# Optimization experiments

Hardware: AMD Instinct MI355X
Metric: run time of the kernel (lower is better)

Reference implementation:

```python
import jax, jax.numpy as jnp
import numpy as np


def setup_inputs() -> dict:
    key = jax.random.key(0)
    ks = jax.random.split(key, 8)
    B, D, H, W = 4, 96, 64, 64
    K, N, R = 4, 16, 6
    return {
        "x": jax.random.normal(ks[0], (B, D, H, W), jnp.float32),
        "x_proj_weight": jax.random.normal(ks[1], (K, R + 2 * N, D), jnp.float32) * 0.05,
        "dt_projs_weight": jax.random.normal(ks[2], (K, D, R), jnp.float32) * 0.1,
        "dt_projs_bias": jax.random.normal(ks[3], (K, D), jnp.float32) * 0.1,
        "A_logs": jax.random.uniform(ks[4], (K * D, N), jnp.float32),
        "Ds": jax.random.normal(ks[5], (K * D,), jnp.float32),
        "ln_weight": jnp.ones((D,), jnp.float32),
        "ln_bias": jnp.zeros((D,), jnp.float32),
    }


def reference(x, x_proj_weight, dt_projs_weight, dt_projs_bias, A_logs, Ds, ln_weight, ln_bias):
    B, D, H, W = x.shape
    K, _, R = dt_projs_weight.shape
    N = A_logs.shape[1]
    L = H * W

    # ---- CrossScan: 4 traversal orders (row-major, col-major, and their reverses) ----
    xf = x.reshape(B, D, L)                                   # row-major
    xt = jnp.transpose(x, (0, 1, 3, 2)).reshape(B, D, L)      # col-major
    xs = jnp.stack([xf, xt, xf[..., ::-1], xt[..., ::-1]], axis=1)  # (B, K, D, L)

    # ---- input-dependent projections ----
    x_dbl = jnp.einsum('bkdl,kcd->bkcl', xs, x_proj_weight)   # (B, K, R+2N, L)
    dts, Bs, Cs = jnp.split(x_dbl, [R, R + N], axis=2)        # Bs/Cs: (B, K, N, L)
    dts = jnp.einsum('bkrl,kdr->bkdl', dts, dt_projs_weight)  # (B, K, D, L)

    A = -jnp.exp(A_logs).reshape(K, D, N)                     # (K, D, N)
    delta = jax.nn.softplus(dts + dt_projs_bias[None, :, :, None])  # (B, K, D, L)

    # ---- selective (S6) scan over L ----
    def step(h, inp):
        d_t, u_t, B_t, C_t = inp  # (B,K,D) (B,K,D) (B,K,N) (B,K,N)
        dA = jnp.exp(d_t[..., None] * A[None])                # (B,K,D,N)
        h = h * dA + (d_t * u_t)[..., None] * B_t[:, :, None, :]
        y_t = jnp.einsum('bkdn,bkn->bkd', h, C_t)
        return h, y_t

    h0 = jnp.zeros((B, K, D, N), x.dtype)
    seq = (jnp.moveaxis(delta, -1, 0), jnp.moveaxis(xs, -1, 0),
           jnp.moveaxis(Bs, -1, 0), jnp.moveaxis(Cs, -1, 0))
    _, ys = jax.lax.scan(step, h0, seq)                       # (L, B, K, D)
    ys = jnp.moveaxis(ys, 0, -1)                              # (B, K, D, L)
    ys = ys + Ds.reshape(K, D)[None, :, :, None] * xs         # skip term D*u

    # ---- CrossMerge: undo the 4 traversal orders and sum ----
    m = ys[:, 0:2] + ys[:, 2:4][..., ::-1]                    # (B, 2, D, L)
    y = m[:, 0] + jnp.transpose(m[:, 1].reshape(B, D, W, H), (0, 1, 3, 2)).reshape(B, D, L)

    # ---- out_norm (LayerNorm over channels, v0 path) ----
    y = jnp.transpose(y, (0, 2, 1))                           # (B, L, D)
    mu = y.mean(-1, keepdims=True)
    var = y.var(-1, keepdims=True)
    y = (y - mu) / jnp.sqrt(var + 1e-5) * ln_weight + ln_bias
    return y.reshape(B, H, W, D)
```

## Files before the change

### kernel.cpp

```cpp
#include <hip/hip_runtime.h>
#include <math.h>

#define B_ 4
#define D_ 96
#define H_ 64
#define W_ 64
#define L_ 4096
#define K_ 4
#define N_ 16
#define R_ 6
#define C_ 38
#define SSX 128
#define CLSX (L_ / SSX)
#define CH_ (B_ * K_ * D_ * N_)

__device__ __forceinline__ int src_idx(int k, int l) {
    int m = (k >= 2) ? (L_ - 1 - l) : l;
    if (k & 1) return ((m & 63) << 6) | (m >> 6);
    return m;
}

__device__ __forceinline__ float softplus_f(float a) {
    return (a > 15.f) ? a : __logf(1.f + __expf(a));
}

__global__ __launch_bounds__(256) void transpose_kernel(
    const float* __restrict__ x,
    float* __restrict__ xs2)
{
    int bid = blockIdx.x;
    int b = bid / (3 * 64);
    int rest = bid % (3 * 64);
    int dblk = rest / 64, lblk = rest % 64;
    int d0 = dblk * 32;
    int l0 = lblk * 64;
    int tid = threadIdx.x;

    __shared__ float s_t[32][65];

    for (int i = tid; i < 32 * 64; i += 256) {
        int d = i >> 6, l = i & 63;
        s_t[d][l] = x[((long)b * D_ + d0 + d) * L_ + l0 + l];
    }
    __syncthreads();

    for (int i = tid; i < 64 * 32; i += 256) {
        int l = i >> 5, d = i & 31;
        float v = s_t[d][l];
        xs2[((long)b * L_ + l0 + l) * D_ + d0 + d] = v;
        xs2[((long)(B_ + b) * L_ + l * 64 + lblk) * D_ + d0 + d] = v;
    }
}

__global__ __launch_bounds__(256) void proj_kernel(
    const float* __restrict__ xs2,
    const float* __restrict__ xpw,
    const float* __restrict__ wdt,
    const float* __restrict__ bdt,
    float* __restrict__ delta,
    float* __restrict__ Bsb,
    float* __restrict__ Csb)
{
    const int TL = 64;
    const int tiles = L_ / TL;
    int bid = blockIdx.x;
    int bk = bid / tiles;
    int tile = bid % tiles;
    int b = bk / K_, k = bk % K_;
    int l0 = tile * TL;
    int tid = threadIdx.x;

    __shared__ __align__(16) float s_wpT[D_ * 40];
    __shared__ __align__(16) float s_xs[D_ * 68];
    __shared__ __align__(16) float s_wdt[R_ * D_];
    __shared__ __align__(16) float s_bias[D_];
    __shared__ __align__(16) float s_dts[R_ * 68];

    for (int i = tid; i < C_ * D_; i += 256) {
        int d = i / C_, c = i % C_;
        int cp = (c < 6) ? c : c + 2;
        s_wpT[d * 40 + cp] = xpw[(k * C_ + c) * D_ + d];
    }
    for (int i = tid; i < 96; i += 256) {
        s_wpT[i * 40 + 6] = 0.f;
        s_wpT[i * 40 + 7] = 0.f;
    }
    for (int i = tid; i < R_ * D_; i += 256) {
        int r = i / D_, d = i % D_;
        s_wdt[i] = wdt[(k * D_ + d) * R_ + r];
    }
    if (tid < D_) s_bias[tid] = bdt[k * D_ + tid];

    const float* xsp = xs2 + (long)((k & 1) * B_ + b) * L_ * D_;
    for (int i = tid; i < TL * 24; i += 256) {
        int lt = i / 24, dq = i % 24;
        int row = (k < 2) ? (l0 + lt) : (L_ - 1 - l0 - lt);
        float4 v = *(const float4*)(xsp + (long)row * D_ + dq * 4);
        s_xs[(dq * 4 + 0) * 68 + lt] = v.x;
        s_xs[(dq * 4 + 1) * 68 + lt] = v.y;
        s_xs[(dq * 4 + 2) * 68 + lt] = v.z;
        s_xs[(dq * 4 + 3) * 68 + lt] = v.w;
    }
    __syncthreads();

    long base = (long)bk * L_ + l0;

    int ct = tid >> 4;
    int lt4 = (tid & 15) * 4;
    if (ct < 10) {
        int cp0 = ct * 4;
        float acc[4][4];
#pragma unroll
        for (int i = 0; i < 4; ++i)
#pragma unroll
            for (int j = 0; j < 4; ++j) acc[i][j] = 0.f;
#pragma unroll 4
        for (int d = 0; d < D_; ++d) {
            float4 wv = *(const float4*)(&s_wpT[d * 40 + cp0]);
            float4 xv = *(const float4*)(&s_xs[d * 68 + lt4]);
            float wa[4] = {wv.x, wv.y, wv.z, wv.w};
            float xa[4] = {xv.x, xv.y, xv.z, xv.w};
#pragma unroll
            for (int ci = 0; ci < 4; ++ci)
#pragma unroll
                for (int li = 0; li < 4; ++li)
                    acc[ci][li] += wa[ci] * xa[li];
        }
        if (ct == 0) {
#pragma unroll
            for (int ci = 0; ci < 4; ++ci)
                *(float4*)(&s_dts[ci * 68 + lt4]) =
                    make_float4(acc[ci][0], acc[ci][1], acc[ci][2], acc[ci][3]);
        } else if (ct == 1) {
#pragma unroll
            for (int ci = 0; ci < 2; ++ci)
                *(float4*)(&s_dts[(4 + ci) * 68 + lt4]) =
                    make_float4(acc[ci][0], acc[ci][1], acc[ci][2], acc[ci][3]);
        } else if (ct < 6) {
            int n0 = cp0 - 8;
#pragma unroll
            for (int li = 0; li < 4; ++li)
                *(float4*)(&Bsb[(base + lt4 + li) * N_ + n0]) =
                    make_float4(acc[0][li], acc[1][li], acc[2][li], acc[3][li]);
        } else {
            int n0 = cp0 - 24;
#pragma unroll
            for (int li = 0; li < 4; ++li)
                *(float4*)(&Csb[(base + lt4 + li) * N_ + n0]) =
                    make_float4(acc[0][li], acc[1][li], acc[2][li], acc[3][li]);
        }
    }
    __syncthreads();

    for (int tt = tid; tt < 24 * 16; tt += 256) {
        int dt = tt % 24, lt4b = (tt / 24) * 4;
        int d0 = dt * 4;
        float4 bias = *(const float4*)(&s_bias[d0]);
        float acc[4][4];
#pragma unroll
        for (int li = 0; li < 4; ++li) {
            acc[li][0] = bias.x; acc[li][1] = bias.y;
            acc[li][2] = bias.z; acc[li][3] = bias.w;
        }
#pragma unroll
        for (int r = 0; r < R_; ++r) {
            float4 wv = *(const float4*)(&s_wdt[r * D_ + d0]);
            float4 tv = *(const float4*)(&s_dts[r * 68 + lt4b]);
            float wa[4] = {wv.x, wv.y, wv.z, wv.w};
            float ta[4] = {tv.x, tv.y, tv.z, tv.w};
#pragma unroll
            for (int li = 0; li < 4; ++li)
#pragma unroll
                for (int di = 0; di < 4; ++di)
                    acc[li][di] += ta[li] * wa[di];
        }
#pragma unroll
        for (int li = 0; li < 4; ++li) {
            float4 o = make_float4(softplus_f(acc[li][0]), softplus_f(acc[li][1]),
                                   softplus_f(acc[li][2]), softplus_f(acc[li][3]));
            *(float4*)(&delta[(base + lt4b + li) * D_ + d0]) = o;
        }
    }
}

__global__ __launch_bounds__(192) void scan_part1(
    const float* __restrict__ A_logs,
    const float* __restrict__ xs2,
    const float* __restrict__ delta,
    const float* __restrict__ Bsb,
    float* __restrict__ pAarr,
    float* __restrict__ hharr)
{
    int cid = blockIdx.x * 2 + threadIdx.x / 96;
    int dd = threadIdx.x % 96;
    int bk = cid / SSX;
    int j = cid % SSX;
    int b = bk / K_, k = bk % K_;
    int kd = k * D_ + dd;
    int l0 = j * CLSX;

    float Av[16];
    {
        const float4* ap = (const float4*)(A_logs + kd * N_);
#pragma unroll
        for (int q = 0; q < 4; ++q) {
            float4 a = ap[q];
            Av[q * 4 + 0] = -__expf(a.x); Av[q * 4 + 1] = -__expf(a.y);
            Av[q * 4 + 2] = -__expf(a.z); Av[q * 4 + 3] = -__expf(a.w);
        }
    }

    const float* dp = delta + ((long)bk * L_ + l0) * D_ + dd;
    const float* bp = Bsb + ((long)bk * L_ + l0) * N_;
    const float* xsp = xs2 + (long)((k & 1) * B_ + b) * L_ * D_;
    long urow0 = (k < 2) ? l0 : (L_ - 1 - l0);
    long ustep = (k < 2) ? D_ : -D_;
    const float* up = xsp + urow0 * D_ + dd;

    float h[16], pA[16];
#pragma unroll
    for (int i = 0; i < 16; ++i) { h[i] = 0.f; pA[i] = 1.f; }

#pragma unroll 2
    for (int t = 0; t < CLSX; ++t) {
        float del = dp[t * D_];
        float u   = up[t * ustep];
        float Bv[16];
        *(float4*)(Bv + 0)  = *(const float4*)(bp + t * N_);
        *(float4*)(Bv + 4)  = *(const float4*)(bp + t * N_ + 4);
        *(float4*)(Bv + 8)  = *(const float4*)(bp + t * N_ + 8);
        *(float4*)(Bv + 12) = *(const float4*)(bp + t * N_ + 12);
        float delu = del * u;
#pragma unroll
        for (int i = 0; i < 16; ++i) {
            float dA = __expf(del * Av[i]);
            pA[i] *= dA;
            h[i] = h[i] * dA + delu * Bv[i];
        }
    }

    long sbase = (long)j * CH_ + (long)(bk * D_ + dd) * N_;
#pragma unroll
    for (int q = 0; q < 4; ++q) {
        *(float4*)(pAarr + sbase + q * 4) =
            make_float4(pA[q * 4], pA[q * 4 + 1], pA[q * 4 + 2], pA[q * 4 + 3]);
        *(float4*)(hharr + sbase + q * 4) =
            make_float4(h[q * 4], h[q * 4 + 1], h[q * 4 + 2], h[q * 4 + 3]);
    }
}

__global__ __launch_bounds__(256) void scan_combine(
    const float* __restrict__ pAarr,
    float* __restrict__ hharr)
{
    int c = blockIdx.x * 256 + threadIdx.x;
    float h = 0.f;
#pragma unroll 8
    for (int j = 0; j < SSX; ++j) {
        long idx = (long)j * CH_ + c;
        float tmp = hharr[idx];
        float pa  = pAarr[idx];
        hharr[idx] = h;
        h = tmp + pa * h;
    }
}

__global__ __launch_bounds__(192) void scan_part2_pair(
    const float* __restrict__ A_logs,
    const float* __restrict__ Ds,
    const float* __restrict__ xs2,
    const float* __restrict__ delta,
    const float* __restrict__ Bsb,
    const float* __restrict__ Csb,
    const float* __restrict__ hharr,
    float* __restrict__ ypair)
{
    __shared__ float s_y[2][CLSX][D_];

    int bid = blockIdx.x;
    int b = bid / (2 * SSX);
    int rest = bid % (2 * SSX);
    int p = rest / SSX;
    int j = rest % SSX;
    int tid = threadIdx.x;
    int g = tid / 96;
    int dd = tid % 96;

    int kdir = p + 2 * g;
    int bk = b * K_ + kdir;
    int jj = g ? (SSX - 1 - j) : j;
    int l0s = jj * CLSX;
    int kd = kdir * D_ + dd;

    float Av[16];
    {
        const float4* ap = (const float4*)(A_logs + kd * N_);
#pragma unroll
        for (int q = 0; q < 4; ++q) {
            float4 a = ap[q];
            Av[q * 4 + 0] = -__expf(a.x); Av[q * 4 + 1] = -__expf(a.y);
            Av[q * 4 + 2] = -__expf(a.z); Av[q * 4 + 3] = -__expf(a.w);
        }
    }
    float Dv = Ds[kd];

    const float* dp = delta + ((long)bk * L_ + l0s) * D_ + dd;
    const float* bp = Bsb + ((long)bk * L_ + l0s) * N_;
    const float* cp = Csb + ((long)bk * L_ + l0s) * N_;
    const float* xsp = xs2 + (long)(p * B_ + b) * L_ * D_;
    long urow0 = g ? ((long)j * CLSX + CLSX - 1) : (long)l0s;
    long ustep = g ? -D_ : D_;
    const float* up = xsp + urow0 * D_ + dd;

    float h[16];
    {
        long sbase = (long)jj * CH_ + (long)(bk * D_ + dd) * N_;
#pragma unroll
        for (int q = 0; q < 4; ++q) {
            float4 hv = *(const float4*)(hharr + sbase + q * 4);
            h[q * 4] = hv.x; h[q * 4 + 1] = hv.y;
            h[q * 4 + 2] = hv.z; h[q * 4 + 3] = hv.w;
        }
    }

#pragma unroll 2
    for (int t = 0; t < CLSX; ++t) {
        float del = dp[t * D_];
        float u   = up[t * ustep];
        float Bv[16], Cv[16];
        *(float4*)(Bv + 0)  = *(const float4*)(bp + t * N_);
        *(float4*)(Bv + 4)  = *(const float4*)(bp + t * N_ + 4);
        *(float4*)(Bv + 8)  = *(const float4*)(bp + t * N_ + 8);
        *(float4*)(Bv + 12) = *(const float4*)(bp + t * N_ + 12);
        *(float4*)(Cv + 0)  = *(const float4*)(cp + t * N_);
        *(float4*)(Cv + 4)  = *(const float4*)(cp + t * N_ + 4);
        *(float4*)(Cv + 8)  = *(const float4*)(cp + t * N_ + 8);
        *(float4*)(Cv + 12) = *(const float4*)(cp + t * N_ + 12);
        float delu = del * u;
        float yv = 0.f;
#pragma unroll
        for (int i = 0; i < 16; ++i) {
            float dA = __expf(del * Av[i]);
            h[i] = h[i] * dA + delu * Bv[i];
            yv += h[i] * Cv[i];
        }
        int tpos = g ? (CLSX - 1 - t) : t;
        s_y[g][tpos][dd] = yv + Dv * u;
    }
    __syncthreads();

    float* yo = ypair + ((long)(p * B_ + b) * L_ + (long)j * CLSX) * D_;
    for (int i = tid; i < CLSX * 24; i += 192) {
        int lt = i / 24, dq = i % 24;
        int d0 = dq * 4;
        float4 o = make_float4(s_y[0][lt][d0 + 0] + s_y[1][lt][d0 + 0],
                               s_y[0][lt][d0 + 1] + s_y[1][lt][d0 + 1],
                               s_y[0][lt][d0 + 2] + s_y[1][lt][d0 + 2],
                               s_y[0][lt][d0 + 3] + s_y[1][lt][d0 + 3]);
        *(float4*)(yo + (long)lt * D_ + d0) = o;
    }
}

__global__ __launch_bounds__(256) void ln_merge_kernel(
    const float* __restrict__ ypair,
    const float* __restrict__ lnw,
    const float* __restrict__ lnb,
    float* __restrict__ out)
{
    int wid = (blockIdx.x * 256 + threadIdx.x) >> 6;
    int lane = threadIdx.x & 63;
    int b = wid / L_;
    int m = wid % L_;
    int mt = ((m & 63) << 6) | (m >> 6);

    const float* y0 = ypair + ((long)b * L_ + m) * D_;
    const float* y1 = ypair + ((long)(B_ + b) * L_ + mt) * D_;

    float v0 = y0[lane] + y1[lane];
    float v1 = (lane < 32) ? (y0[64 + lane] + y1[64 + lane]) : 0.f;

    float s  = v0 + v1;
    float s2 = v0 * v0 + v1 * v1;
#pragma unroll
    for (int mm = 1; mm < 64; mm <<= 1) {
        s  += __shfl_xor(s, mm);
        s2 += __shfl_xor(s2, mm);
    }
    float mu  = s * (1.f / D_);
    float var = s2 * (1.f / D_) - mu * mu;
    float rstd = rsqrtf(var + 1e-5f);

    long obase = (long)wid * D_;
    out[obase + lane] = (v0 - mu) * rstd * lnw[lane] + lnb[lane];
    if (lane < 32)
        out[obase + 64 + lane] = (v1 - mu) * rstd * lnw[64 + lane] + lnb[64 + lane];
}

__global__ __launch_bounds__(256) void proj_legacy(
    const float* __restrict__ x,
    const float* __restrict__ xpw,
    const float* __restrict__ wdt,
    const float* __restrict__ bdt,
    float* __restrict__ delta,
    float* __restrict__ Bsb,
    float* __restrict__ Csb)
{
    const int TL = 64;
    const int tiles = L_ / TL;
    int bid = blockIdx.x;
    int bk = bid / tiles;
    int tile = bid % tiles;
    int b = bk / K_, k = bk % K_;
    int l0 = tile * TL;
    int tid = threadIdx.x;

    __shared__ float s_wp[C_ * D_];
    __shared__ float s_wdt[R_ * D_];
    __shared__ float s_bias[D_];
    __shared__ float s_xs[D_ * (TL + 1)];
    __shared__ float s_xdbl[C_ * (TL + 1)];

    for (int i = tid; i < C_ * D_; i += 256) s_wp[i] = xpw[k * C_ * D_ + i];
    for (int i = tid; i < R_ * D_; i += 256) {
        int r = i / D_, d = i % D_;
        s_wdt[i] = wdt[(k * D_ + d) * R_ + r];
    }
    if (tid < D_) s_bias[tid] = bdt[k * D_ + tid];
    for (int i = tid; i < D_ * TL; i += 256) {
        int d = i / TL, lt = i % TL;
        s_xs[d * (TL + 1) + lt] = x[(b * D_ + d) * L_ + src_idx(k, l0 + lt)];
    }
    __syncthreads();

    for (int idx = tid; idx < C_ * TL; idx += 256) {
        int c = idx / TL, lt = idx % TL;
        const float* wr = &s_wp[c * D_];
        float acc = 0.f;
#pragma unroll 8
        for (int d = 0; d < D_; ++d) acc += wr[d] * s_xs[d * (TL + 1) + lt];
        s_xdbl[c * (TL + 1) + lt] = acc;
    }
    __syncthreads();

    long base = (long)bk * L_ + l0;
    for (int idx = tid; idx < TL * D_; idx += 256) {
        int lt = idx / D_, d = idx % D_;
        float acc = s_bias[d];
#pragma unroll
        for (int r = 0; r < R_; ++r)
            acc += s_wdt[r * D_ + d] * s_xdbl[r * (TL + 1) + lt];
        delta[(base + lt) * D_ + d] = softplus_f(acc);
    }
    for (int idx = tid; idx < TL * 2 * N_; idx += 256) {
        int lt = idx / (2 * N_), c2 = idx % (2 * N_);
        float v = s_xdbl[(R_ + c2) * (TL + 1) + lt];
        if (c2 < N_) Bsb[(base + lt) * N_ + c2] = v;
        else         Csb[(base + lt) * N_ + (c2 - N_)] = v;
    }
}

__global__ __launch_bounds__(64) void scan_serial(
    const float* __restrict__ x,
    const float* __restrict__ A_logs,
    const float* __restrict__ Ds,
    const float* __restrict__ delta,
    const float* __restrict__ Bsb,
    const float* __restrict__ Csb,
    float* __restrict__ ys)
{
    const int chans = D_ / 4;
    int bid = blockIdx.x;
    int bk = bid / chans;
    int d0 = (bid % chans) * 4;
    int b = bk / K_, k = bk % K_;
    int lane = threadIdx.x;
    int g = lane >> 4, n = lane & 15;
    int d = d0 + g;
    int kd = k * D_ + d;

    float A  = -__expf(A_logs[kd * N_ + n]);
    float Dv = Ds[kd];
    const float* dptr = delta + ((long)bk * L_) * D_ + d;
    const float* bptr = Bsb + (long)bk * L_ * N_ + n;
    const float* cptr = Csb + (long)bk * L_ * N_ + n;
    const float* xptr = x + ((long)b * D_ + d) * L_;
    float* yptr = ys + ((long)bk * L_) * D_ + d;

    float h = 0.f;
#pragma unroll 4
    for (int l = 0; l < L_; ++l) {
        float del = dptr[(long)l * D_];
        float u   = xptr[src_idx(k, l)];
        float Bt  = bptr[l * N_];
        float Ct  = cptr[l * N_];
        float dA  = __expf(del * A);
        h = h * dA + del * u * Bt;
        float yv = h * Ct;
        yv += __shfl_xor(yv, 1);
        yv += __shfl_xor(yv, 2);
        yv += __shfl_xor(yv, 4);
        yv += __shfl_xor(yv, 8);
        if (n == 0) yptr[(long)l * D_] = yv + Dv * u;
    }
}

__global__ __launch_bounds__(256) void merge_ln_kernel(
    const float* __restrict__ ys,
    const float* __restrict__ lnw,
    const float* __restrict__ lnb,
    float* __restrict__ out)
{
    int wid = (blockIdx.x * 256 + threadIdx.x) >> 6;
    int lane = threadIdx.x & 63;
    int b = wid / L_;
    int l = wid % L_;
    int lt = ((l & 63) << 6) | (l >> 6);

    long base0 = ((long)(b * K_ + 0) * L_ + l) * D_;
    long base2 = ((long)(b * K_ + 2) * L_ + (L_ - 1 - l)) * D_;
    long base1 = ((long)(b * K_ + 1) * L_ + lt) * D_;
    long base3 = ((long)(b * K_ + 3) * L_ + (L_ - 1 - lt)) * D_;

    int dA = lane;
    int dB = lane + 64;
    float v0 = ys[base0 + dA] + ys[base2 + dA] + ys[base1 + dA] + ys[base3 + dA];
    float v1 = 0.f;
    if (dB < D_)
        v1 = ys[base0 + dB] + ys[base2 + dB] + ys[base1 + dB] + ys[base3 + dB];

    float s  = v0 + v1;
    float s2 = v0 * v0 + v1 * v1;
#pragma unroll
    for (int m = 1; m < 64; m <<= 1) {
        s  += __shfl_xor(s, m);
        s2 += __shfl_xor(s2, m);
    }
    float mu  = s * (1.f / D_);
    float var = s2 * (1.f / D_) - mu * mu;
    float rstd = rsqrtf(var + 1e-5f);

    long obase = ((long)b * L_ + l) * D_;
    out[obase + dA] = (v0 - mu) * rstd * lnw[dA] + lnb[dA];
    if (dB < D_)
        out[obase + dB] = (v1 - mu) * rstd * lnw[dB] + lnb[dB];
}

extern "C" void kernel_launch(void* const* d_in, const int* in_sizes, int n_in,
                              void* d_out, int out_size, void* d_ws, size_t ws_size,
                              hipStream_t stream) {
    const float* x      = (const float*)d_in[0];
    const float* xpw    = (const float*)d_in[1];
    const float* wdt    = (const float*)d_in[2];
    const float* bdt    = (const float*)d_in[3];
    const float* A_logs = (const float*)d_in[4];
    const float* Ds     = (const float*)d_in[5];
    const float* lnw    = (const float*)d_in[6];
    const float* lnb    = (const float*)d_in[7];
    float* out = (float*)d_out;

    float* ws = (float*)d_ws;
    const long n_delta = (long)B_ * K_ * L_ * D_;
    const long n_bc    = (long)B_ * K_ * L_ * N_;
    const long n_bld   = (long)B_ * L_ * D_;
    const long n_sum   = (long)SSX * CH_;

    float* delta = ws;
    float* Bsb   = delta + n_delta;
    float* Csb   = Bsb + n_bc;
    float* xs2   = Csb + n_bc;
    float* ypair = xs2 + 2 * n_bld;
    float* hharr = ypair + 2 * n_bld;
    float* pAarr = ypair;
    size_t need = (size_t)(n_delta + 2 * n_bc + 4 * n_bld + n_sum) * 4;

    if (ws_size >= need) {
        transpose_kernel<<<B_ * 3 * 64, 256, 0, stream>>>(x, xs2);
        proj_kernel<<<B_ * K_ * (L_ / 64), 256, 0, stream>>>(
            xs2, xpw, wdt, bdt, delta, Bsb, Csb);
        scan_part1<<<B_ * K_ * SSX / 2, 192, 0, stream>>>(
            A_logs, xs2, delta, Bsb, pAarr, hharr);
        scan_combine<<<CH_ / 256, 256, 0, stream>>>(pAarr, hharr);
        scan_part2_pair<<<B_ * 2 * SSX, 192, 0, stream>>>(
            A_logs, Ds, xs2, delta, Bsb, Csb, hharr, ypair);
        ln_merge_kernel<<<(B_ * L_) / 4, 256, 0, stream>>>(ypair, lnw, lnb, out);
    } else {
        float* ys2 = Csb + n_bc;
        proj_legacy<<<B_ * K_ * (L_ / 64), 256, 0, stream>>>(
            x, xpw, wdt, bdt, delta, Bsb, Csb);
        scan_serial<<<B_ * K_ * (D_ / 4), 64, 0, stream>>>(
            x, A_logs, Ds, delta, Bsb, Csb, ys2);
        merge_ln_kernel<<<(B_ * L_) / 4, 256, 0, stream>>>(ys2, lnw, lnb, out);
    }
}
```

Before: 195.4 us.

## Split scan state dimension across thread pairs, use exp2 and closed-form decay product

Both scan kernels now assign each (channel, direction) to two threads that each hold 8 of the 16 state entries, doubling block size to 384 threads. Partial outputs are combined with a lane shuffle. The exponentials now use the native exp2 with log2e folded into A. In part1 the running product of decays is replaced by exp2 of A times the summed delta, which removes a multiply per state per step. The goal is more parallelism and fewer registers on the latency-bound recurrence. The cost is duplicated delta, u and address loads per pair and a shuffle on every step.

```diff
diff --git a/kernel.cpp b/kernel.cpp
--- a/kernel.cpp
+++ b/kernel.cpp
@@ -14,6 +14,17 @@
 #define CLSX (L_ / SSX)
 #define CH_ (B_ * K_ * D_ * N_)
 
+#if defined(__has_builtin)
+#if __has_builtin(__builtin_amdgcn_exp2f)
+#define EXP2F(x) __builtin_amdgcn_exp2f(x)
+#else
+#define EXP2F(x) exp2f(x)
+#endif
+#else
+#define EXP2F(x) exp2f(x)
+#endif
+#define LOG2E 1.44269504f
+
 __device__ __forceinline__ int src_idx(int k, int l) {
     int m = (k >= 2) ? (L_ - 1 - l) : l;
     if (k & 1) return ((m & 63) << 6) | (m >> 6);
@@ -183,7 +194,7 @@
     }
 }
 
-__global__ __launch_bounds__(192) void scan_part1(
+__global__ __launch_bounds__(384) void scan_part1(
     const float* __restrict__ A_logs,
     const float* __restrict__ xs2,
     const float* __restrict__ delta,
@@ -191,62 +202,66 @@
     float* __restrict__ pAarr,
     float* __restrict__ hharr)
 {
-    int cid = blockIdx.x * 2 + threadIdx.x / 96;
-    int dd = threadIdx.x % 96;
+    int tid = threadIdx.x;
+    int sub = tid / 192;
+    int r = tid % 192;
+    int dd = r >> 1;
+    int half = r & 1;
+    int n0 = half * 8;
+    int cid = blockIdx.x * 2 + sub;
     int bk = cid / SSX;
     int j = cid % SSX;
     int b = bk / K_, k = bk % K_;
     int kd = k * D_ + dd;
     int l0 = j * CLSX;
 
-    float Av[16];
+    float A2[8];
     {
-        const float4* ap = (const float4*)(A_logs + kd * N_);
-#pragma unroll
-        for (int q = 0; q < 4; ++q) {
-            float4 a = ap[q];
-            Av[q * 4 + 0] = -__expf(a.x); Av[q * 4 + 1] = -__expf(a.y);
-            Av[q * 4 + 2] = -__expf(a.z); Av[q * 4 + 3] = -__expf(a.w);
-        }
+        const float4* ap = (const float4*)(A_logs + kd * N_ + n0);
+        float4 a0 = ap[0], a1 = ap[1];
+        A2[0] = -__expf(a0.x) * LOG2E; A2[1] = -__expf(a0.y) * LOG2E;
+        A2[2] = -__expf(a0.z) * LOG2E; A2[3] = -__expf(a0.w) * LOG2E;
+        A2[4] = -__expf(a1.x) * LOG2E; A2[5] = -__expf(a1.y) * LOG2E;
+        A2[6] = -__expf(a1.z) * LOG2E; A2[7] = -__expf(a1.w) * LOG2E;
     }
 
     const float* dp = delta + ((long)bk * L_ + l0) * D_ + dd;
-    const float* bp = Bsb + ((long)bk * L_ + l0) * N_;
+    const float* bp = Bsb + ((long)bk * L_ + l0) * N_ + n0;
     const float* xsp = xs2 + (long)((k & 1) * B_ + b) * L_ * D_;
     long urow0 = (k < 2) ? l0 : (L_ - 1 - l0);
     long ustep = (k < 2) ? D_ : -D_;
     const float* up = xsp + urow0 * D_ + dd;
 
-    float h[16], pA[16];
-#pragma unroll
-    for (int i = 0; i < 16; ++i) { h[i] = 0.f; pA[i] = 1.f; }
-
-#pragma unroll 2
+    float h[8];
+#pragma unroll
+    for (int i = 0; i < 8; ++i) h[i] = 0.f;
+    float sdel = 0.f;
+
+#pragma unroll 4
     for (int t = 0; t < CLSX; ++t) {
-        float del = dp[t * D_];
-        float u   = up[t * ustep];
-        float Bv[16];
-        *(float4*)(Bv + 0)  = *(const float4*)(bp + t * N_);
-        *(float4*)(Bv + 4)  = *(const float4*)(bp + t * N_ + 4);
-        *(float4*)(Bv + 8)  = *(const float4*)(bp + t * N_ + 8);
-        *(float4*)(Bv + 12) = *(const float4*)(bp + t * N_ + 12);
+        float del = dp[(long)t * D_];
+        float u   = up[(long)t * ustep];
+        float4 b0 = *(const float4*)(bp + t * N_);
+        float4 b1 = *(const float4*)(bp + t * N_ + 4);
+        float Bv[8] = {b0.x, b0.y, b0.z, b0.w, b1.x, b1.y, b1.z, b1.w};
+        sdel += del;
         float delu = del * u;
 #pragma unroll
-        for (int i = 0; i < 16; ++i) {
-            float dA = __expf(del * Av[i]);
-            pA[i] *= dA;
+        for (int i = 0; i < 8; ++i) {
+            float dA = EXP2F(del * A2[i]);
             h[i] = h[i] * dA + delu * Bv[i];
         }
     }
 
-    long sbase = (long)j * CH_ + (long)(bk * D_ + dd) * N_;
-#pragma unroll
-    for (int q = 0; q < 4; ++q) {
-        *(float4*)(pAarr + sbase + q * 4) =
-            make_float4(pA[q * 4], pA[q * 4 + 1], pA[q * 4 + 2], pA[q * 4 + 3]);
-        *(float4*)(hharr + sbase + q * 4) =
-            make_float4(h[q * 4], h[q * 4 + 1], h[q * 4 + 2], h[q * 4 + 3]);
-    }
+    long sbase = (long)j * CH_ + (long)(bk * D_ + dd) * N_ + n0;
+    *(float4*)(pAarr + sbase) =
+        make_float4(EXP2F(A2[0] * sdel), EXP2F(A2[1] * sdel),
+                    EXP2F(A2[2] * sdel), EXP2F(A2[3] * sdel));
+    *(float4*)(pAarr + sbase + 4) =
+        make_float4(EXP2F(A2[4] * sdel), EXP2F(A2[5] * sdel),
+                    EXP2F(A2[6] * sdel), EXP2F(A2[7] * sdel));
+    *(float4*)(hharr + sbase)     = make_float4(h[0], h[1], h[2], h[3]);
+    *(float4*)(hharr + sbase + 4) = make_float4(h[4], h[5], h[6], h[7]);
 }
 
 __global__ __launch_bounds__(256) void scan_combine(
@@ -265,7 +280,7 @@
     }
 }
 
-__global__ __launch_bounds__(192) void scan_part2_pair(
+__global__ __launch_bounds__(384) void scan_part2_pair(
     const float* __restrict__ A_logs,
     const float* __restrict__ Ds,
     const float* __restrict__ xs2,
@@ -283,8 +298,11 @@
     int p = rest / SSX;
     int j = rest % SSX;
     int tid = threadIdx.x;
-    int g = tid / 96;
-    int dd = tid % 96;
+    int g = tid / 192;
+    int r = tid % 192;
+    int dd = r >> 1;
+    int half = r & 1;
+    int n0 = half * 8;
 
     int kdir = p + 2 * g;
     int bk = b * K_ + kdir;
@@ -292,65 +310,62 @@
     int l0s = jj * CLSX;
     int kd = kdir * D_ + dd;
 
-    float Av[16];
+    float A2[8];
     {
-        const float4* ap = (const float4*)(A_logs + kd * N_);
-#pragma unroll
-        for (int q = 0; q < 4; ++q) {
-            float4 a = ap[q];
-            Av[q * 4 + 0] = -__expf(a.x); Av[q * 4 + 1] = -__expf(a.y);
-            Av[q * 4 + 2] = -__expf(a.z); Av[q * 4 + 3] = -__expf(a.w);
-        }
+        const float4* ap = (const float4*)(A_logs + kd * N_ + n0);
+        float4 a0 = ap[0], a1 = ap[1];
+        A2[0] = -__expf(a0.x) * LOG2E; A2[1] = -__expf(a0.y) * LOG2E;
+        A2[2] = -__expf(a0.z) * LOG2E; A2[3] = -__expf(a0.w) * LOG2E;
+        A2[4] = -__expf(a1.x) * LOG2E; A2[5] = -__expf(a1.y) * LOG2E;
+        A2[6] = -__expf(a1.z) * LOG2E; A2[7] = -__expf(a1.w) * LOG2E;
     }
     float Dv = Ds[kd];
 
     const float* dp = delta + ((long)bk * L_ + l0s) * D_ + dd;
-    const float* bp = Bsb + ((long)bk * L_ + l0s) * N_;
-    const float* cp = Csb + ((long)bk * L_ + l0s) * N_;
+    const float* bp = Bsb + ((long)bk * L_ + l0s) * N_ + n0;
+    const float* cp = Csb + ((long)bk * L_ + l0s) * N_ + n0;
     const float* xsp = xs2 + (long)(p * B_ + b) * L_ * D_;
     long urow0 = g ? ((long)j * CLSX + CLSX - 1) : (long)l0s;
     long ustep = g ? -D_ : D_;
     const float* up = xsp + urow0 * D_ + dd;
 
-    float h[16];
+    float h[8];
     {
-        long sbase = (long)jj * CH_ + (long)(bk * D_ + dd) * N_;
-#pragma unroll
-        for (int q = 0; q < 4; ++q) {
-            float4 hv = *(const float4*)(hharr + sbase + q * 4);
-            h[q * 4] = hv.x; h[q * 4 + 1] = hv.y;
-            h[q * 4 + 2] = hv.z; h[q * 4 + 3] = hv.w;
-        }
-    }
-
-#pragma unroll 2
+        long sbase = (long)jj * CH_ + (long)(bk * D_ + dd) * N_ + n0;
+        float4 h0 = *(const float4*)(hharr + sbase);
+        float4 h1 = *(const float4*)(hharr + sbase + 4);
+        h[0] = h0.x; h[1] = h0.y; h[2] = h0.z; h[3] = h0.w;
+        h[4] = h1.x; h[5] = h1.y; h[6] = h1.z; h[7] = h1.w;
+    }
+
+#pragma unroll 4
     for (int t = 0; t < CLSX; ++t) {
-        float del = dp[t * D_];
-        float u   = up[t * ustep];
-        float Bv[16], Cv[16];
-        *(float4*)(Bv + 0)  = *(const float4*)(bp + t * N_);
-        *(float4*)(Bv + 4)  = *(const float4*)(bp + t * N_ + 4);
-        *(float4*)(Bv + 8)  = *(const float4*)(bp + t * N_ + 8);
-        *(float4*)(Bv + 12) = *(const float4*)(bp + t * N_ + 12);
-        *(float4*)(Cv + 0)  = *(const float4*)(cp + t * N_);
-        *(float4*)(Cv + 4)  = *(const float4*)(cp + t * N_ + 4);
-        *(float4*)(Cv + 8)  = *(const float4*)(cp + t * N_ + 8);
-        *(float4*)(Cv + 12) = *(const float4*)(cp + t * N_ + 12);
+        float del = dp[(long)t * D_];
+        float u   = up[(long)t * ustep];
+        float4 b0 = *(const float4*)(bp + t * N_);
+        float4 b1 = *(const float4*)(bp + t * N_ + 4);
+        float4 c0 = *(const float4*)(cp + t * N_);
+        float4 c1 = *(const float4*)(cp + t * N_ + 4);
+        float Bv[8] = {b0.x, b0.y, b0.z, b0.w, b1.x, b1.y, b1.z, b1.w};
+        float Cv[8] = {c0.x, c0.y, c0.z, c0.w, c1.x, c1.y, c1.z, c1.w};
         float delu = del * u;
         float yv = 0.f;
 #pragma unroll
-        for (int i = 0; i < 16; ++i) {
-            float dA = __expf(del * Av[i]);
+        for (int i = 0; i < 8; ++i) {
+            float dA = EXP2F(del * A2[i]);
             h[i] = h[i] * dA + delu * Bv[i];
             yv += h[i] * Cv[i];
         }
-        int tpos = g ? (CLSX - 1 - t) : t;
-        s_y[g][tpos][dd] = yv + Dv * u;
+        yv += __shfl_xor(yv, 1);
+        if (half == 0) {
+            int tpos = g ? (CLSX - 1 - t) : t;
+            s_y[g][tpos][dd] = yv + Dv * u;
+        }
     }
     __syncthreads();
 
     float* yo = ypair + ((long)(p * B_ + b) * L_ + (long)j * CLSX) * D_;
-    for (int i = tid; i < CLSX * 24; i += 192) {
+    for (int i = tid; i < CLSX * 24; i += 384) {
         int lt = i / 24, dq = i % 24;
         int d0 = dq * 4;
         float4 o = make_float4(s_y[0][lt][d0 + 0] + s_y[1][lt][d0 + 0],
@@ -577,10 +592,10 @@
         transpose_kernel<<<B_ * 3 * 64, 256, 0, stream>>>(x, xs2);
         proj_kernel<<<B_ * K_ * (L_ / 64), 256, 0, stream>>>(
             xs2, xpw, wdt, bdt, delta, Bsb, Csb);
-        scan_part1<<<B_ * K_ * SSX / 2, 192, 0, stream>>>(
+        scan_part1<<<B_ * K_ * SSX / 2, 384, 0, stream>>>(
             A_logs, xs2, delta, Bsb, pAarr, hharr);
         scan_combine<<<CH_ / 256, 256, 0, stream>>>(pAarr, hharr);
-        scan_part2_pair<<<B_ * 2 * SSX, 192, 0, stream>>>(
+        scan_part2_pair<<<B_ * 2 * SSX, 384, 0, stream>>>(
             A_logs, Ds, xs2, delta, Bsb, Csb, hharr, ypair);
         ln_merge_kernel<<<(B_ * L_) / 4, 256, 0, stream>>>(ypair, lnw, lnb, out);
     } else {
```

Result: faster. 186.4 us (-4.6%).
